# Performance work log

Hardware: AMD Instinct MI355X
Metric: run time of the kernel (lower is better)

## Reference

```python
import jax, jax.numpy as jnp
import numpy as np

N, NFEAT, OUT, NREL = 4096, 128, 64, 7


def setup_inputs() -> dict:
    key = jax.random.key(0)
    ks = jax.random.split(key, 12)
    mask = jax.random.uniform(ks[0], (NREL, N, N)) < 0.01
    vals = jax.random.uniform(ks[1], (NREL, N, N))
    A_stack = jnp.where(mask, vals, 0.0).astype(jnp.float32)
    feature = jax.random.normal(ks[2], (N, NFEAT), jnp.float32)
    encode = (jax.random.uniform(ks[3], (N, NREL)) < 0.3).astype(jnp.float32)
    stdv = 1.0 / np.sqrt(OUT)
    W1 = jax.random.uniform(ks[4], (NFEAT, OUT), jnp.float32, -stdv, stdv)
    b1 = jax.random.uniform(ks[5], (OUT,), jnp.float32, -stdv, stdv)
    W2 = jax.random.uniform(ks[6], (OUT, OUT), jnp.float32, -stdv, stdv)
    b2 = jax.random.uniform(ks[7], (OUT,), jnp.float32, -stdv, stdv)
    weight_b = jax.random.uniform(ks[8], (NREL, 1), jnp.float32, 0.0, 0.1)
    relation_interaction = 0.1 * jax.random.normal(ks[9], (3, 3), jnp.float32)
    interaction_strength = jnp.array([0.5], jnp.float32)
    struct_weight = jax.random.uniform(ks[10], (NREL,), jnp.float32, 0.0, 0.1)
    return dict(feature=feature, A_stack=A_stack, encode=encode, W1=W1, b1=b1,
                W2=W2, b2=b2, weight_b=weight_b,
                relation_interaction=relation_interaction,
                interaction_strength=interaction_strength,
                struct_weight=struct_weight)


def _l2_normalize(x):
    norm = jnp.clip(jnp.linalg.norm(x, axis=1, keepdims=True), 1e-12)
    return x / norm


def _gcn(x, adj, W, b):
    # torch.mm(input, weight) then torch.spmm(adj, support) + bias
    return adj @ (x @ W) + b


def reference(feature, A_stack, encode, W1, b1, W2, b2, weight_b,
              relation_interaction, interaction_strength, struct_weight):
    # adj_matrix_weight_merge: weighted sum of 7 relation adjacencies, symmetrized
    merged = jnp.einsum('rnm,r->nm', A_stack, weight_b[:, 0])  # [N,N]
    bbp_A = merged + merged.T

    # relation-interaction enhancement over the first 3 relations (i != j)
    R = A_stack[:3]  # [3,N,N]
    M = relation_interaction * (1.0 - jnp.eye(3, dtype=relation_interaction.dtype))
    mult = jnp.einsum('ij,inm,jnm->nm', M, R, R)                       # coeff*Ri*Rj
    cond = jnp.einsum('ij,inm,jnm->nm', M, (R > 0).astype(R.dtype), R)  # coeff*(Ri>0)*Rj
    interaction_A = jnp.tanh(0.6 * mult + 0.4 * cond)

    final_A = bbp_A + interaction_strength[0] * interaction_A

    U1 = _gcn(feature, final_A, W1, b1)
    U2 = _gcn(U1, final_A, W2, b2)

    # construct_adj(encode, struct_weight): weighted structural similarity
    struct_adj = (encode * struct_weight) @ encode.T  # [N,N]
    U3 = _gcn(feature, struct_adj, W1, b1)
    U4 = _gcn(U3, struct_adj, W2, b2)

    branch1 = (U1 + U2) / 2
    result = (branch1 + U4) / 2
    branch2 = U4
    return (_l2_normalize(result), _l2_normalize(branch1), _l2_normalize(branch2))
```

## Files before the change

### kernel.cpp

```cpp
#include <hip/hip_runtime.h>
#include <math.h>

#define NDIM 4096
#define NNSZ ((size_t)NDIM*(size_t)NDIM)

typedef __attribute__((ext_vector_type(8))) short short8;
typedef __attribute__((ext_vector_type(4))) float f32x4;

__device__ __forceinline__ unsigned short f2bf(float x) {
  unsigned u = __float_as_uint(x);
  u += 0x7FFFu + ((u >> 16) & 1u);
  return (unsigned short)(u >> 16);
}
__device__ __forceinline__ float bf2f(unsigned short u) {
  return __uint_as_float(((unsigned)u) << 16);
}

__device__ __forceinline__ float inter_term(float r0, float r1, float r2,
    float m01, float m02, float m10, float m12, float m20, float m21) {
  float mult = (m01 + m10) * (r0 * r1) + (m02 + m20) * (r0 * r2) + (m12 + m21) * (r1 * r2);
  float i0 = (r0 > 0.f) ? 1.f : 0.f;
  float i1 = (r1 > 0.f) ? 1.f : 0.f;
  float i2 = (r2 > 0.f) ? 1.f : 0.f;
  float cond = m01 * i0 * r1 + m02 * i0 * r2
             + m10 * i1 * r0 + m12 * i1 * r2
             + m20 * i2 * r0 + m21 * i2 * r1;
  float a = 0.6f * mult + 0.4f * cond;
  return (a == 0.0f) ? 0.0f : tanhf(a);
}

__global__ __launch_bounds__(256) void k_pass1(
    const float* __restrict__ A, const float* __restrict__ wb,
    const float* __restrict__ Mri, const float* __restrict__ strength,
    unsigned short* __restrict__ P, unsigned short* __restrict__ Mm)
{
  const int row = blockIdx.x;
  const int tid = threadIdx.x;
  const size_t rowoff = (size_t)row * NDIM;

  float w[7];
#pragma unroll
  for (int r = 0; r < 7; ++r) w[r] = wb[r];
  const float m01 = Mri[1], m02 = Mri[2], m10 = Mri[3];
  const float m12 = Mri[5], m20 = Mri[6], m21 = Mri[7];
  const float s = strength[0];

#pragma unroll
  for (int q = 0; q < 4; ++q) {
    const size_t off = rowoff + (size_t)(q * 1024) + tid * 4;
    float4 v[7];
#pragma unroll
    for (int r = 0; r < 7; ++r)
      v[r] = *(const float4*)(A + (size_t)r * NNSZ + off);

    float4 acc = make_float4(0.f, 0.f, 0.f, 0.f);
#pragma unroll
    for (int r = 0; r < 7; ++r) {
      acc.x = fmaf(w[r], v[r].x, acc.x);
      acc.y = fmaf(w[r], v[r].y, acc.y);
      acc.z = fmaf(w[r], v[r].z, acc.z);
      acc.w = fmaf(w[r], v[r].w, acc.w);
    }
    float t0 = inter_term(v[0].x, v[1].x, v[2].x, m01, m02, m10, m12, m20, m21);
    float t1 = inter_term(v[0].y, v[1].y, v[2].y, m01, m02, m10, m12, m20, m21);
    float t2 = inter_term(v[0].z, v[1].z, v[2].z, m01, m02, m10, m12, m20, m21);
    float t3 = inter_term(v[0].w, v[1].w, v[2].w, m01, m02, m10, m12, m20, m21);

    *(ushort4*)(Mm + off) = make_ushort4(f2bf(acc.x), f2bf(acc.y), f2bf(acc.z), f2bf(acc.w));
    *(ushort4*)(P + off)  = make_ushort4(f2bf(fmaf(s, t0, acc.x)), f2bf(fmaf(s, t1, acc.y)),
                                         f2bf(fmaf(s, t2, acc.z)), f2bf(fmaf(s, t3, acc.w)));
  }
}

__global__ __launch_bounds__(256) void k_pass2(
    const unsigned short* __restrict__ P, const unsigned short* __restrict__ Mm,
    unsigned short* __restrict__ F)
{
  const int bi = blockIdx.x, bj = blockIdx.y;
  __shared__ unsigned short t[64 * 65];
  const int x  = threadIdx.x >> 2;
  const int y0 = (threadIdx.x & 3) << 4;

  const size_t moff = (size_t)(bj * 64 + x) * NDIM + bi * 64 + y0;
  unsigned short mv[16];
  ((uint4*)mv)[0] = *(const uint4*)(Mm + moff);
  ((uint4*)mv)[1] = *(const uint4*)(Mm + moff + 8);
#pragma unroll
  for (int e = 0; e < 16; ++e) t[x * 65 + y0 + e] = mv[e];
  __syncthreads();

  const size_t off = (size_t)(bi * 64 + x) * NDIM + bj * 64 + y0;
  unsigned short pv[16], ov[16];
  ((uint4*)pv)[0] = *(const uint4*)(P + off);
  ((uint4*)pv)[1] = *(const uint4*)(P + off + 8);
#pragma unroll
  for (int e = 0; e < 16; ++e)
    ov[e] = f2bf(bf2f(pv[e]) + bf2f(t[(y0 + e) * 65 + x]));
  *(uint4*)(F + off)     = ((const uint4*)ov)[0];
  *(uint4*)(F + off + 8) = ((const uint4*)ov)[1];
}

__global__ __launch_bounds__(64) void k_z1(const float* __restrict__ feat,
    const float* __restrict__ W1, float* __restrict__ Z1) {
  int n = blockIdx.x, j = threadIdx.x;
  __shared__ float fr[128];
  fr[j] = feat[n * 128 + j];
  fr[j + 64] = feat[n * 128 + 64 + j];
  __syncthreads();
  float acc = 0.f;
#pragma unroll 8
  for (int k = 0; k < 128; ++k) acc = fmaf(fr[k], W1[k * 64 + j], acc);
  Z1[(size_t)n * 64 + j] = acc;
}

__global__ __launch_bounds__(256) void k_transpose_bf16(
    const float* __restrict__ Z, unsigned short* __restrict__ Zt) {
  __shared__ float tile[64][65];
  const int n0 = blockIdx.x * 64;
  const int c = threadIdx.x & 63;
  const int r0 = threadIdx.x >> 6;
#pragma unroll
  for (int i = 0; i < 16; ++i) {
    int r = r0 * 16 + i;
    tile[r][c] = Z[(size_t)(n0 + r) * 64 + c];
  }
  __syncthreads();
#pragma unroll
  for (int i = 0; i < 16; ++i) {
    int j = r0 * 16 + i;
    Zt[(size_t)j * NDIM + n0 + c] = f2bf(tile[c][j]);
  }
}

__global__ __launch_bounds__(512) void k_mfma_gemm(
    const unsigned short* __restrict__ Fb,
    const unsigned short* __restrict__ Zt,
    const float* __restrict__ bias,
    float* __restrict__ U)
{
  __shared__ float red[8][16][66];
  const int strip = blockIdx.x * 16;
  const int w = threadIdx.x >> 6;
  const int lane = threadIdx.x & 63;
  const int arow = lane & 15;
  const int kq = lane >> 4;
  const int k_base = w * 512;

  f32x4 acc[4] = {};
  const unsigned short* Ap  = Fb + (size_t)(strip + arow) * NDIM + k_base + kq * 8;
  const unsigned short* Bp0 = Zt + (size_t)(arow) * NDIM + k_base + kq * 8;
  const unsigned short* Bp1 = Bp0 + (size_t)16 * NDIM;
  const unsigned short* Bp2 = Bp0 + (size_t)32 * NDIM;
  const unsigned short* Bp3 = Bp0 + (size_t)48 * NDIM;

#pragma unroll 4
  for (int step = 0; step < 16; ++step) {
    const int k0 = step * 32;
    short8 a  = *(const short8*)(Ap  + k0);
    short8 b0 = *(const short8*)(Bp0 + k0);
    short8 b1v = *(const short8*)(Bp1 + k0);
    short8 b2v = *(const short8*)(Bp2 + k0);
    short8 b3v = *(const short8*)(Bp3 + k0);
    acc[0] = __builtin_amdgcn_mfma_f32_16x16x32_bf16(a, b0,  acc[0], 0, 0, 0);
    acc[1] = __builtin_amdgcn_mfma_f32_16x16x32_bf16(a, b1v, acc[1], 0, 0, 0);
    acc[2] = __builtin_amdgcn_mfma_f32_16x16x32_bf16(a, b2v, acc[2], 0, 0, 0);
    acc[3] = __builtin_amdgcn_mfma_f32_16x16x32_bf16(a, b3v, acc[3], 0, 0, 0);
  }
#pragma unroll
  for (int t = 0; t < 4; ++t)
#pragma unroll
    for (int r = 0; r < 4; ++r)
      red[w][kq * 4 + r][t * 16 + arow] = acc[t][r];
  __syncthreads();

  const int col = threadIdx.x & 63;
  const int row0 = threadIdx.x >> 6;
#pragma unroll
  for (int rr = 0; rr < 2; ++rr) {
    const int row = row0 + rr * 8;
    float sum = 0.f;
#pragma unroll
    for (int ww = 0; ww < 8; ++ww) sum += red[ww][row][col];
    U[(size_t)(strip + row) * 64 + col] = sum + bias[col];
  }
}

__device__ __forceinline__ float wave_sum64(float v) {
#pragma unroll
  for (int o = 32; o > 0; o >>= 1) v += __shfl_xor(v, o, 64);
  return v;
}

__global__ __launch_bounds__(512) void k_gemm2f(
    const unsigned short* __restrict__ Fb,
    const unsigned short* __restrict__ Zt,
    const float* __restrict__ b2,
    const float* __restrict__ U1,
    const float* __restrict__ encode,
    const float* __restrict__ sw,
    const float* __restrict__ G2,
    float* __restrict__ out)
{
  __shared__ float red[8][16][66];
  const int strip = blockIdx.x * 16;
  const int w = threadIdx.x >> 6;
  const int lane = threadIdx.x & 63;
  const int arow = lane & 15;
  const int kq = lane >> 4;
  const int k_base = w * 512;

  f32x4 acc[4] = {};
  const unsigned short* Ap  = Fb + (size_t)(strip + arow) * NDIM + k_base + kq * 8;
  const unsigned short* Bp0 = Zt + (size_t)(arow) * NDIM + k_base + kq * 8;
  const unsigned short* Bp1 = Bp0 + (size_t)16 * NDIM;
  const unsigned short* Bp2 = Bp0 + (size_t)32 * NDIM;
  const unsigned short* Bp3 = Bp0 + (size_t)48 * NDIM;

#pragma unroll 4
  for (int step = 0; step < 16; ++step) {
    const int k0 = step * 32;
    short8 a  = *(const short8*)(Ap  + k0);
    short8 b0 = *(const short8*)(Bp0 + k0);
    short8 b1v = *(const short8*)(Bp1 + k0);
    short8 b2v = *(const short8*)(Bp2 + k0);
    short8 b3v = *(const short8*)(Bp3 + k0);
    acc[0] = __builtin_amdgcn_mfma_f32_16x16x32_bf16(a, b0,  acc[0], 0, 0, 0);
    acc[1] = __builtin_amdgcn_mfma_f32_16x16x32_bf16(a, b1v, acc[1], 0, 0, 0);
    acc[2] = __builtin_amdgcn_mfma_f32_16x16x32_bf16(a, b2v, acc[2], 0, 0, 0);
    acc[3] = __builtin_amdgcn_mfma_f32_16x16x32_bf16(a, b3v, acc[3], 0, 0, 0);
  }
#pragma unroll
  for (int t = 0; t < 4; ++t)
#pragma unroll
    for (int r = 0; r < 4; ++r)
      red[w][kq * 4 + r][t * 16 + arow] = acc[t][r];
  __syncthreads();

  const int col = threadIdx.x & 63;
  const int row0 = threadIdx.x >> 6;
#pragma unroll
  for (int rr = 0; rr < 2; ++rr) {
    const int row = row0 + rr * 8;
    const int n = strip + row;
    float sum = 0.f;
#pragma unroll
    for (int ww = 0; ww < 8; ++ww) sum += red[ww][row][col];
    float u2 = sum + b2[col];
    float u1 = U1[(size_t)n * 64 + col];
    float br = 0.5f * (u1 + u2);
    float u4 = b2[col];
#pragma unroll
    for (int r = 0; r < 7; ++r)
      u4 = fmaf(encode[n * 7 + r] * sw[r], G2[r * 64 + col], u4);
    float rs = 0.5f * (br + u4);
    float nr = fmaxf(sqrtf(wave_sum64(rs * rs)), 1e-12f);
    float nb = fmaxf(sqrtf(wave_sum64(br * br)), 1e-12f);
    float nu = fmaxf(sqrtf(wave_sum64(u4 * u4)), 1e-12f);
    size_t idx = (size_t)n * 64 + col;
    out[idx] = rs / nr;
    out[(size_t)NDIM * 64 + idx] = br / nb;
    out[2 * (size_t)NDIM * 64 + idx] = u4 / nu;
  }
}

__global__ __launch_bounds__(256) void k_z2t(const float* __restrict__ U1,
    const float* __restrict__ W2, unsigned short* __restrict__ Z2t) {
  __shared__ float W2s[64][65];
  const int n0 = blockIdx.x * 64;
  const int j = threadIdx.x & 63;
  const int g = threadIdx.x >> 6;
  for (int r = g; r < 64; r += 4) W2s[r][j] = W2[r * 64 + j];
  __syncthreads();
  float acc[16];
#pragma unroll
  for (int r = 0; r < 16; ++r) acc[r] = 0.f;
  const float* Urow = U1 + (size_t)(n0 + g * 16) * 64;
  for (int k = 0; k < 64; ++k) {
    float wv = W2s[k][j];
#pragma unroll
    for (int r = 0; r < 16; ++r) acc[r] = fmaf(Urow[r * 64 + k], wv, acc[r]);
  }
  unsigned short ov[16];
#pragma unroll
  for (int r = 0; r < 16; ++r) ov[r] = f2bf(acc[r]);
  *(uint4*)(Z2t + (size_t)j * NDIM + n0 + g * 16)     = *(const uint4*)&ov[0];
  *(uint4*)(Z2t + (size_t)j * NDIM + n0 + g * 16 + 8) = *(const uint4*)&ov[8];
}

__global__ __launch_bounds__(512) void k_zero_small(float* __restrict__ g) {
  int t = threadIdx.x;
  if (t < 448) g[t] = 0.f;
}

__global__ __launch_bounds__(256) void k_sc(const float* __restrict__ encode,
    const float* __restrict__ sw, float* __restrict__ S, float* __restrict__ c) {
  __shared__ float red[4][56];
  float sl[49], cl[7];
#pragma unroll
  for (int i = 0; i < 49; ++i) sl[i] = 0.f;
#pragma unroll
  for (int i = 0; i < 7; ++i) cl[i] = 0.f;
  for (int n = threadIdx.x; n < NDIM; n += 256) {
    float e[7];
#pragma unroll
    for (int r = 0; r < 7; ++r) e[r] = encode[n * 7 + r];
#pragma unroll
    for (int i = 0; i < 7; ++i) {
      cl[i] += e[i];
#pragma unroll
      for (int j = 0; j < 7; ++j) sl[i * 7 + j] = fmaf(e[i], e[j], sl[i * 7 + j]);
    }
  }
  const int lane = threadIdx.x & 63;
  const int w = threadIdx.x >> 6;
#pragma unroll
  for (int i = 0; i < 49; ++i) {
#pragma unroll
    for (int o = 32; o > 0; o >>= 1) sl[i] += __shfl_xor(sl[i], o, 64);
  }
#pragma unroll
  for (int i = 0; i < 7; ++i) {
#pragma unroll
    for (int o = 32; o > 0; o >>= 1) cl[i] += __shfl_xor(cl[i], o, 64);
  }
  if (lane == 0) {
#pragma unroll
    for (int i = 0; i < 49; ++i) red[w][i] = sl[i];
#pragma unroll
    for (int i = 0; i < 7; ++i) red[w][49 + i] = cl[i];
  }
  __syncthreads();
  if (threadIdx.x < 49)
    S[threadIdx.x] = (red[0][threadIdx.x] + red[1][threadIdx.x] + red[2][threadIdx.x] + red[3][threadIdx.x]) * sw[threadIdx.x % 7];
  if (threadIdx.x >= 49 && threadIdx.x < 56) {
    int i = threadIdx.x;
    c[i - 49] = red[0][i] + red[1][i] + red[2][i] + red[3][i];
  }
}

__global__ __launch_bounds__(256) void k_g1(const float* __restrict__ encode,
    const float* __restrict__ Z1, float* __restrict__ G1) {
  const int j = threadIdx.x & 63;
  const int grp = threadIdx.x >> 6;
  const int n0 = blockIdx.x * 128 + grp * 32;
  float acc[7];
#pragma unroll
  for (int r = 0; r < 7; ++r) acc[r] = 0.f;
  for (int i = 0; i < 32; ++i) {
    int n = n0 + i;
    float z = Z1[(size_t)n * 64 + j];
#pragma unroll
    for (int r = 0; r < 7; ++r) acc[r] = fmaf(encode[n * 7 + r], z, acc[r]);
  }
#pragma unroll
  for (int r = 0; r < 7; ++r) atomicAdd(&G1[r * 64 + j], acc[r]);
}

__global__ __launch_bounds__(64) void k_g2(const float* __restrict__ S,
    const float* __restrict__ c, const float* __restrict__ G1,
    const float* __restrict__ W2, const float* __restrict__ b1,
    float* __restrict__ G2) {
  int j = threadIdx.x;
  float h = 0.f;
  for (int k = 0; k < 64; ++k) h = fmaf(b1[k], W2[k * 64 + j], h);
  float gw[7];
#pragma unroll
  for (int r = 0; r < 7; ++r) {
    float v = 0.f;
    for (int k = 0; k < 64; ++k) v = fmaf(G1[r * 64 + k], W2[k * 64 + j], v);
    gw[r] = v;
  }
#pragma unroll
  for (int r = 0; r < 7; ++r) {
    float v = c[r] * h;
#pragma unroll
    for (int q = 0; q < 7; ++q) v = fmaf(S[r * 7 + q], gw[q], v);
    G2[r * 64 + j] = v;
  }
}

extern "C" void kernel_launch(void* const* d_in, const int* in_sizes, int n_in,
                              void* d_out, int out_size, void* d_ws, size_t ws_size,
                              hipStream_t stream) {
  const float* feature  = (const float*)d_in[0];
  const float* A        = (const float*)d_in[1];
  const float* encode   = (const float*)d_in[2];
  const float* W1       = (const float*)d_in[3];
  const float* b1       = (const float*)d_in[4];
  const float* W2       = (const float*)d_in[5];
  const float* b2       = (const float*)d_in[6];
  const float* wb       = (const float*)d_in[7];
  const float* Mri      = (const float*)d_in[8];
  const float* strength = (const float*)d_in[9];
  const float* sw       = (const float*)d_in[10];
  float* out = (float*)d_out;

  const size_t NV = (size_t)NDIM * 64;
  unsigned short* P  = (unsigned short*)d_ws;
  unsigned short* Mm = P + NNSZ;
  unsigned short* Fb = Mm + NNSZ;
  float* Z1 = (float*)(Fb + NNSZ);
  float* U1 = Z1 + NV;
  float* U2 = U1 + NV;
  unsigned short* Z1t = (unsigned short*)(U2 + NV);
  unsigned short* Z2t = Z1t + NV;
  float* G1 = (float*)(Z2t + NV);
  float* S  = G1 + 448;
  float* c  = S + 49;
  float* G2 = c + 7;

  hipLaunchKernelGGL(k_zero_small, dim3(1), dim3(512), 0, stream, G1);
  hipLaunchKernelGGL(k_pass1, dim3(NDIM), dim3(256), 0, stream, A, wb, Mri, strength, P, Mm);
  hipLaunchKernelGGL(k_pass2, dim3(64, 64), dim3(256), 0, stream, P, Mm, Fb);
  hipLaunchKernelGGL(k_z1, dim3(NDIM), dim3(64), 0, stream, feature, W1, Z1);
  hipLaunchKernelGGL(k_transpose_bf16, dim3(64), dim3(256), 0, stream, Z1, Z1t);
  hipLaunchKernelGGL(k_sc, dim3(1), dim3(256), 0, stream, encode, sw, S, c);
  hipLaunchKernelGGL(k_g1, dim3(32), dim3(256), 0, stream, encode, Z1, G1);
  hipLaunchKernelGGL(k_g2, dim3(1), dim3(64), 0, stream, S, c, G1, W2, b1, G2);
  hipLaunchKernelGGL(k_mfma_gemm, dim3(NDIM / 16), dim3(512), 0, stream, Fb, Z1t, b1, U1);
  hipLaunchKernelGGL(k_z2t, dim3(64), dim3(256), 0, stream, U1, W2, Z2t);
  hipLaunchKernelGGL(k_gemm2f, dim3(NDIM / 16), dim3(512), 0, stream, Fb, Z2t, b2, U1, encode, sw, G2, out);
}
```

Before: 247.3 us.

## Store relation-interaction term sparsely and apply it in a fix-up kernel

The pass-1 kernel no longer writes a dense bf16 P matrix. It evaluates the tanh interaction term only where at least two of the first three relations are nonzero, which are the only entries where it can be nonzero. Those entries go into a capped index/value list through an atomic counter, and a new kernel adds them into the final bf16 matrix after the transpose-add pass. This removes a full N×N bf16 write plus most tanh work, and pass 2 now reads Mm twice instead of reading P. The costs are an extra launch, atomics, a different bf16 rounding order, and silently dropped entries if the count exceeds the 262144 cap.

```diff
diff --git a/kernel.cpp b/kernel.cpp
--- a/kernel.cpp
+++ b/kernel.cpp
@@ -3,6 +3,7 @@
 
 #define NDIM 4096
 #define NNSZ ((size_t)NDIM*(size_t)NDIM)
+#define SCAP 262144u
 
 typedef __attribute__((ext_vector_type(8))) short short8;
 typedef __attribute__((ext_vector_type(4))) float f32x4;
@@ -32,7 +33,8 @@
 __global__ __launch_bounds__(256) void k_pass1(
     const float* __restrict__ A, const float* __restrict__ wb,
     const float* __restrict__ Mri, const float* __restrict__ strength,
-    unsigned short* __restrict__ P, unsigned short* __restrict__ Mm)
+    unsigned short* __restrict__ Mm, unsigned* __restrict__ sidx,
+    float* __restrict__ sval, unsigned* __restrict__ scnt)
 {
   const int row = blockIdx.x;
   const int tid = threadIdx.x;
@@ -61,20 +63,45 @@
       acc.z = fmaf(w[r], v[r].z, acc.z);
       acc.w = fmaf(w[r], v[r].w, acc.w);
     }
-    float t0 = inter_term(v[0].x, v[1].x, v[2].x, m01, m02, m10, m12, m20, m21);
-    float t1 = inter_term(v[0].y, v[1].y, v[2].y, m01, m02, m10, m12, m20, m21);
-    float t2 = inter_term(v[0].z, v[1].z, v[2].z, m01, m02, m10, m12, m20, m21);
-    float t3 = inter_term(v[0].w, v[1].w, v[2].w, m01, m02, m10, m12, m20, m21);
-
     *(ushort4*)(Mm + off) = make_ushort4(f2bf(acc.x), f2bf(acc.y), f2bf(acc.z), f2bf(acc.w));
-    *(ushort4*)(P + off)  = make_ushort4(f2bf(fmaf(s, t0, acc.x)), f2bf(fmaf(s, t1, acc.y)),
-                                         f2bf(fmaf(s, t2, acc.z)), f2bf(fmaf(s, t3, acc.w)));
+
+    {
+      float r0 = v[0].x, r1 = v[1].x, r2 = v[2].x;
+      if ((int)(r0 != 0.f) + (int)(r1 != 0.f) + (int)(r2 != 0.f) >= 2) {
+        float t = inter_term(r0, r1, r2, m01, m02, m10, m12, m20, m21);
+        unsigned idx = atomicAdd(scnt, 1u);
+        if (idx < SCAP) { sidx[idx] = (unsigned)(off + 0); sval[idx] = s * t; }
+      }
+    }
+    {
+      float r0 = v[0].y, r1 = v[1].y, r2 = v[2].y;
+      if ((int)(r0 != 0.f) + (int)(r1 != 0.f) + (int)(r2 != 0.f) >= 2) {
+        float t = inter_term(r0, r1, r2, m01, m02, m10, m12, m20, m21);
+        unsigned idx = atomicAdd(scnt, 1u);
+        if (idx < SCAP) { sidx[idx] = (unsigned)(off + 1); sval[idx] = s * t; }
+      }
+    }
+    {
+      float r0 = v[0].z, r1 = v[1].z, r2 = v[2].z;
+      if ((int)(r0 != 0.f) + (int)(r1 != 0.f) + (int)(r2 != 0.f) >= 2) {
+        float t = inter_term(r0, r1, r2, m01, m02, m10, m12, m20, m21);
+        unsigned idx = atomicAdd(scnt, 1u);
+        if (idx < SCAP) { sidx[idx] = (unsigned)(off + 2); sval[idx] = s * t; }
+      }
+    }
+    {
+      float r0 = v[0].w, r1 = v[1].w, r2 = v[2].w;
+      if ((int)(r0 != 0.f) + (int)(r1 != 0.f) + (int)(r2 != 0.f) >= 2) {
+        float t = inter_term(r0, r1, r2, m01, m02, m10, m12, m20, m21);
+        unsigned idx = atomicAdd(scnt, 1u);
+        if (idx < SCAP) { sidx[idx] = (unsigned)(off + 3); sval[idx] = s * t; }
+      }
+    }
   }
 }
 
 __global__ __launch_bounds__(256) void k_pass2(
-    const unsigned short* __restrict__ P, const unsigned short* __restrict__ Mm,
-    unsigned short* __restrict__ F)
+    const unsigned short* __restrict__ Mm, unsigned short* __restrict__ F)
 {
   const int bi = blockIdx.x, bj = blockIdx.y;
   __shared__ unsigned short t[64 * 65];
@@ -91,13 +118,24 @@
 
   const size_t off = (size_t)(bi * 64 + x) * NDIM + bj * 64 + y0;
   unsigned short pv[16], ov[16];
-  ((uint4*)pv)[0] = *(const uint4*)(P + off);
-  ((uint4*)pv)[1] = *(const uint4*)(P + off + 8);
+  ((uint4*)pv)[0] = *(const uint4*)(Mm + off);
+  ((uint4*)pv)[1] = *(const uint4*)(Mm + off + 8);
 #pragma unroll
   for (int e = 0; e < 16; ++e)
     ov[e] = f2bf(bf2f(pv[e]) + bf2f(t[(y0 + e) * 65 + x]));
   *(uint4*)(F + off)     = ((const uint4*)ov)[0];
   *(uint4*)(F + off + 8) = ((const uint4*)ov)[1];
+}
+
+__global__ __launch_bounds__(256) void k_fix(const unsigned* __restrict__ sidx,
+    const float* __restrict__ sval, const unsigned* __restrict__ scnt,
+    unsigned short* __restrict__ F) {
+  unsigned n = *scnt;
+  if (n > SCAP) n = SCAP;
+  for (unsigned i = blockIdx.x * 256 + threadIdx.x; i < n; i += gridDim.x * 256) {
+    unsigned pos = sidx[i];
+    F[pos] = f2bf(bf2f(F[pos]) + sval[i]);
+  }
 }
 
 __global__ __launch_bounds__(64) void k_z1(const float* __restrict__ feat,
@@ -287,9 +325,11 @@
   *(uint4*)(Z2t + (size_t)j * NDIM + n0 + g * 16 + 8) = *(const uint4*)&ov[8];
 }
 
-__global__ __launch_bounds__(512) void k_zero_small(float* __restrict__ g) {
+__global__ __launch_bounds__(512) void k_zero_small(float* __restrict__ g,
+    unsigned* __restrict__ scnt) {
   int t = threadIdx.x;
   if (t < 448) g[t] = 0.f;
+  if (t == 448) *scnt = 0u;
 }
 
 __global__ __launch_bounds__(256) void k_sc(const float* __restrict__ encode,
@@ -396,8 +436,10 @@
   float* out = (float*)d_out;
 
   const size_t NV = (size_t)NDIM * 64;
-  unsigned short* P  = (unsigned short*)d_ws;
-  unsigned short* Mm = P + NNSZ;
+  unsigned* sidx = (unsigned*)d_ws;
+  float* sval = (float*)(sidx + SCAP);
+  unsigned* scnt = (unsigned*)(sval + SCAP);
+  unsigned short* Mm = (unsigned short*)d_ws + NNSZ;
   unsigned short* Fb = Mm + NNSZ;
   float* Z1 = (float*)(Fb + NNSZ);
   float* U1 = Z1 + NV;
@@ -409,9 +451,10 @@
   float* c  = S + 49;
   float* G2 = c + 7;
 
-  hipLaunchKernelGGL(k_zero_small, dim3(1), dim3(512), 0, stream, G1);
-  hipLaunchKernelGGL(k_pass1, dim3(NDIM), dim3(256), 0, stream, A, wb, Mri, strength, P, Mm);
-  hipLaunchKernelGGL(k_pass2, dim3(64, 64), dim3(256), 0, stream, P, Mm, Fb);
+  hipLaunchKernelGGL(k_zero_small, dim3(1), dim3(512), 0, stream, G1, scnt);
+  hipLaunchKernelGGL(k_pass1, dim3(NDIM), dim3(256), 0, stream, A, wb, Mri, strength, Mm, sidx, sval, scnt);
+  hipLaunchKernelGGL(k_pass2, dim3(64, 64), dim3(256), 0, stream, Mm, Fb);
+  hipLaunchKernelGGL(k_fix, dim3(32), dim3(256), 0, stream, sidx, sval, scnt, Fb);
   hipLaunchKernelGGL(k_z1, dim3(NDIM), dim3(64), 0, stream, feature, W1, Z1);
   hipLaunchKernelGGL(k_transpose_bf16, dim3(64), dim3(256), 0, stream, Z1, Z1t);
   hipLaunchKernelGGL(k_sc, dim3(1), dim3(256), 0, stream, encode, sw, S, c);
```

Measured after the change: 243.2 us. Within noise of the previous version (-1.7%).
